# Kernel optimization log

Measured on AMD Instinct MI355X. Metric: run time of the kernel, lower is better.

The kernel has to match this reference:

```python
import jax, jax.numpy as jnp
import numpy as np

D_MODEL = 512
HEAD = 64

def setup_inputs() -> dict:
    key = jax.random.key(0)
    ks = jax.random.split(key, 7)
    s_in = 1.0 / np.sqrt(D_MODEL)
    x = jax.random.normal(ks[0], (4, 4096, D_MODEL), dtype=jnp.float32)
    Wk = jax.random.uniform(ks[1], (D_MODEL, HEAD), jnp.float32, -s_in, s_in)
    bk = jax.random.uniform(ks[2], (HEAD,), jnp.float32, -s_in, s_in)
    Wq = jax.random.uniform(ks[3], (D_MODEL, HEAD), jnp.float32, -s_in, s_in)
    bq = jax.random.uniform(ks[4], (HEAD,), jnp.float32, -s_in, s_in)
    Wv = jax.random.uniform(ks[5], (D_MODEL, HEAD), jnp.float32, -s_in, s_in)
    bv = jax.random.uniform(ks[6], (HEAD,), jnp.float32, -s_in, s_in)
    return {"x": x, "Wk": Wk, "bk": bk, "Wq": Wq, "bq": bq, "Wv": Wv, "bv": bv}

def reference(x, Wk, bk, Wq, bq, Wv, bv):
    B, T, C = x.shape
    k = x @ Wk + bk            # [B,T,H]
    q = x @ Wq + bq            # [B,T,H]
    v = x @ Wv + bv            # [B,T,H]
    scale = C ** (-0.5)
    # NOTE: original computes k @ q^T (keys index rows), softmax over query axis
    w = jnp.einsum('bkh,bqh->bkq', k, q) * scale  # [B,T,T]
    w = jax.nn.softmax(w, axis=-1)
    out = jnp.einsum('bkq,bqh->bkh', w, v)        # [B,T,H]
    return out
```

## Files before the change

### kernel.cpp

```cpp
#include <hip/hip_runtime.h>


#define DM 512
#define HD 64
#define TSEQ 4096
#define KSCALE (1.4426950408889634f * 0.04419417382415922f)

typedef __attribute__((ext_vector_type(8))) __bf16 bf16x8;
typedef __attribute__((ext_vector_type(4))) __bf16 bf16x4;
typedef __attribute__((ext_vector_type(2))) __bf16 bf16x2;
typedef __attribute__((ext_vector_type(4))) float f32x4;
typedef __attribute__((ext_vector_type(16))) float f32x16;
typedef __attribute__((ext_vector_type(4))) unsigned int uint4v;

__device__ __forceinline__ float fast_exp2(float x) {
#if __has_builtin(__builtin_amdgcn_exp2f)
    return __builtin_amdgcn_exp2f(x);
#else
    return exp2f(x);
#endif
}

__device__ __forceinline__ bf16x8 ld_bf16x8(const unsigned short* p) {
    return __builtin_bit_cast(bf16x8, *(const uint4v*)p);
}
__device__ __forceinline__ f32x4 mfma16(bf16x8 a, bf16x8 b, f32x4 c) {
    return __builtin_amdgcn_mfma_f32_16x16x32_bf16(a, b, c, 0, 0, 0);
}
__device__ __forceinline__ f32x16 mfma32(bf16x8 a, bf16x8 b, f32x16 c) {
    return __builtin_amdgcn_mfma_f32_32x32x16_bf16(a, b, c, 0, 0, 0);
}

typedef const __attribute__((address_space(1))) unsigned int* gas_t;
typedef __attribute__((address_space(3))) unsigned int* las_t;
__device__ __forceinline__ void async_cp16(const void* g, void* l) {
    __builtin_amdgcn_global_load_lds((gas_t)(unsigned long long)g,
                                     (las_t)(unsigned int)(unsigned long long)l,
                                     16, 0, 0);
}

__global__ __launch_bounds__(256) void prep_wt(const float* __restrict__ Wk,
                                               const float* __restrict__ Wq,
                                               const float* __restrict__ Wv,
                                               unsigned short* __restrict__ WT) {
    int e = blockIdx.x * 256 + threadIdx.x;
    int m = e >> 15;
    int idx = e & 32767;
    int h = idx >> 9;
    int cc = idx & 511;
    const float* W = (m == 0) ? Wk : ((m == 1) ? Wq : Wv);
    float v = W[cc * HD + h];
    if (m == 0) v *= KSCALE;
    ((__bf16*)WT)[m * 32768 + h * DM + cc] = (__bf16)v;
}

__global__ __launch_bounds__(512, 4) void proj(const float* __restrict__ x,
                                               const unsigned short* __restrict__ WT,
                                               const float* __restrict__ bk,
                                               const float* __restrict__ bq,
                                               const float* __restrict__ bv,
                                               unsigned short* __restrict__ Kw,
                                               unsigned short* __restrict__ Qw,
                                               unsigned short* __restrict__ VTw) {
    __shared__ alignas(16) float xs[16384];
    const int tid = threadIdx.x;
    const int wv = tid >> 6, lane = tid & 63;
    const int c = lane & 15, quad = lane >> 4;
    const int ng = wv & 3, rg = wv >> 2;
    const int bx = blockIdx.x;
    const int n0 = ng * 16;

#pragma unroll
    for (int r = 0; r < 8; ++r) {
        int cid = r * 512 + tid;
        int row = cid >> 7, pos = cid & 127;
        int g = (pos & ~7) | ((pos ^ row) & 7);
        async_cp16((const char*)x + (size_t)(bx * 32 + row) * 2048 + g * 16,
                   (char*)xs + r * 8192 + wv * 1024);
    }
    __builtin_amdgcn_s_waitcnt(0x0f70);
    __syncthreads();

    const int arow = rg * 16 + c;
    const unsigned short* wtb = WT + (n0 + c) * DM + quad * 8;
    f32x4 acc[3];
#pragma unroll
    for (int m = 0; m < 3; ++m) acc[m] = (f32x4){0.f, 0.f, 0.f, 0.f};

#pragma unroll
    for (int ks = 0; ks < 16; ++ks) {
        int p0 = ks * 8 + quad * 2;
        int sp0 = (p0 & ~7) | ((p0 ^ arow) & 7);
        int sp1 = ((p0 + 1) & ~7) | (((p0 + 1) ^ arow) & 7);
        f32x4 xa = *(const f32x4*)((const char*)xs + arow * 2048 + sp0 * 16);
        f32x4 xb = *(const f32x4*)((const char*)xs + arow * 2048 + sp1 * 16);
        bf16x8 af;
        af[0] = (__bf16)xa[0]; af[1] = (__bf16)xa[1]; af[2] = (__bf16)xa[2]; af[3] = (__bf16)xa[3];
        af[4] = (__bf16)xb[0]; af[5] = (__bf16)xb[1]; af[6] = (__bf16)xb[2]; af[7] = (__bf16)xb[3];
#pragma unroll
        for (int m = 0; m < 3; ++m) {
            bf16x8 bf = ld_bf16x8(wtb + m * 32768 + ks * 32);
            acc[m] = mfma16(af, bf, acc[m]);
        }
    }

    const int row0 = bx * 32 + rg * 16 + quad * 4;
#pragma unroll
    for (int m = 0; m < 3; ++m) {
        const float* bp = (m == 0) ? bk : ((m == 1) ? bq : bv);
        float bias = bp[n0 + c];
        if (m == 0) bias *= KSCALE;
        if (m < 2) {
            __bf16* dst = (__bf16*)((m == 0) ? Kw : Qw);
#pragma unroll
            for (int r = 0; r < 4; ++r)
                dst[(row0 + r) * HD + n0 + c] = (__bf16)(acc[m][r] + bias);
        } else {
            bf16x4 pk;
#pragma unroll
            for (int r = 0; r < 4; ++r) pk[r] = (__bf16)(acc[m][r] + bias);
            int b = bx >> 7;
            int rowb = (bx & 127) * 32 + rg * 16 + quad * 4;
            *(bf16x4*)(VTw + ((size_t)(b * 64 + n0 + c)) * TSEQ + rowb) = pk;
        }
    }
}

__global__ __launch_bounds__(512, 2) void attn(const unsigned short* __restrict__ Kw,
                                               const unsigned short* __restrict__ Qw,
                                               const unsigned short* __restrict__ VTw,
                                               float* __restrict__ Op,
                                               float* __restrict__ Lp) {
    __shared__ alignas(16) char smem[131072];

    const int tid = threadIdx.x;
    const int wv = tid >> 6, lane = tid & 63;
    const int l5 = lane >> 5, l31 = lane & 31;
    const int rg = wv >> 2, jc = wv & 3;
    const int bx = blockIdx.x;
    const int lb = (bx & 7) * 32 + (bx >> 3);
    const int batch = lb >> 6, js = (lb >> 5) & 1, tile = lb & 31;
    const int rowbase = batch * TSEQ + tile * 128;

    bf16x8 kf[2][4];
#pragma unroll
    for (int it = 0; it < 2; ++it) {
        const unsigned short* kp = Kw + (size_t)(rowbase + rg * 64 + it * 32 + l31) * HD;
#pragma unroll
        for (int ks = 0; ks < 4; ++ks) kf[it][ks] = ld_bf16x8(kp + ks * 16 + l5 * 8);
    }

    char* wbase = smem + wv * 16384;

    int qoff[4];
#pragma unroll
    for (int ks = 0; ks < 4; ++ks)
        qoff[ks] = l31 * 128 + (((ks * 2 + l5) ^ (l31 & 7)) * 16);
    int voff[2][2];
#pragma unroll
    for (int ht = 0; ht < 2; ++ht)
#pragma unroll
        for (int k2 = 0; k2 < 2; ++k2) {
            int h = ht * 32 + l31;
            int k = k2 * 2 + l5;
            voff[ht][k2] = h * 64 + (((k + h) & 3) * 16);
        }

    const char* qg = (const char*)(Qw + ((size_t)batch * TSEQ + js * 2048 + jc * 32) * HD);
    const char* vg = (const char*)(VTw + (size_t)batch * 64 * TSEQ) + js * 4096 + jc * 64;
    int qo[4], vo[4];
    {
        const int kk = ((lane & 3) + 4 - ((lane >> 2) & 3)) & 3;
#pragma unroll
        for (int op = 0; op < 4; ++op) {
            int r = (lane >> 3) + 8 * op;
            qo[op] = r * 128 + (((lane & 7) ^ (lane >> 3)) * 16);
            vo[op] = ((lane >> 2) + 16 * op) * 8192 + kk * 16;
        }
    }

    f32x16 o00, o01, o10, o11;
#pragma unroll
    for (int r = 0; r < 16; ++r) { o00[r] = 0.f; o01[r] = 0.f; o10[r] = 0.f; o11[r] = 0.f; }
    float lac0 = 0.f, lac1 = 0.f;

    auto STAGE = [&](int t) {
        char* nb = wbase + (t & 1) * 8192;
#pragma unroll
        for (int op = 0; op < 4; ++op)
            async_cp16(qg + t * 16384 + qo[op], nb + op * 1024);
#pragma unroll
        for (int op = 0; op < 4; ++op)
            async_cp16(vg + t * 256 + vo[op], nb + 4096 + op * 1024);
    };

    auto COMPUTE = [&](int jt) {
        const char* cb = wbase + (jt & 1) * 8192;
        const unsigned short* QL = (const unsigned short*)cb;
        const unsigned short* VL = (const unsigned short*)(cb + 4096);

        f32x16 s0, s1;
#pragma unroll
        for (int r = 0; r < 16; ++r) { s0[r] = 0.f; s1[r] = 0.f; }
#pragma unroll
        for (int ks = 0; ks < 4; ++ks) {
            bf16x8 qa = ld_bf16x8((const unsigned short*)((const char*)QL + qoff[ks]));
            s0 = mfma32(qa, kf[0][ks], s0);
            s1 = mfma32(qa, kf[1][ks], s1);
        }

        unsigned int pk0[8], pk1[8];
#pragma unroll
        for (int m = 0; m < 8; ++m) {
            float a0 = fast_exp2(s0[2 * m]), a1 = fast_exp2(s0[2 * m + 1]);
            float b0 = fast_exp2(s1[2 * m]), b1 = fast_exp2(s1[2 * m + 1]);
            lac0 += a0 + a1;
            lac1 += b0 + b1;
            bf16x2 ta; ta[0] = (__bf16)a0; ta[1] = (__bf16)a1;
            bf16x2 tb; tb[0] = (__bf16)b0; tb[1] = (__bf16)b1;
            pk0[m] = __builtin_bit_cast(unsigned int, ta);
            pk1[m] = __builtin_bit_cast(unsigned int, tb);
        }

#pragma unroll
        for (int k2 = 0; k2 < 2; ++k2) {
            bf16x8 pb0, pb1;
            {
                unsigned int A0 = pk0[k2 * 4 + 0], A1 = pk0[k2 * 4 + 1];
                unsigned int B0 = pk0[k2 * 4 + 2], B1 = pk0[k2 * 4 + 3];
                unsigned int t0 = l5 ? A0 : B0, t1 = l5 ? A1 : B1;
                unsigned int r0 = (unsigned int)__shfl_xor((int)t0, 32, 64);
                unsigned int r1 = (unsigned int)__shfl_xor((int)t1, 32, 64);
                uint4v u;
                u[0] = l5 ? r0 : A0; u[1] = l5 ? r1 : A1;
                u[2] = l5 ? B0 : r0; u[3] = l5 ? B1 : r1;
                pb0 = __builtin_bit_cast(bf16x8, u);
            }
            {
                unsigned int A0 = pk1[k2 * 4 + 0], A1 = pk1[k2 * 4 + 1];
                unsigned int B0 = pk1[k2 * 4 + 2], B1 = pk1[k2 * 4 + 3];
                unsigned int t0 = l5 ? A0 : B0, t1 = l5 ? A1 : B1;
                unsigned int r0 = (unsigned int)__shfl_xor((int)t0, 32, 64);
                unsigned int r1 = (unsigned int)__shfl_xor((int)t1, 32, 64);
                uint4v u;
                u[0] = l5 ? r0 : A0; u[1] = l5 ? r1 : A1;
                u[2] = l5 ? B0 : r0; u[3] = l5 ? B1 : r1;
                pb1 = __builtin_bit_cast(bf16x8, u);
            }
            bf16x8 vf0 = ld_bf16x8((const unsigned short*)((const char*)VL + voff[0][k2]));
            bf16x8 vf1 = ld_bf16x8((const unsigned short*)((const char*)VL + voff[1][k2]));
            o00 = mfma32(vf0, pb0, o00);
            o01 = mfma32(vf0, pb1, o01);
            o10 = mfma32(vf1, pb0, o10);
            o11 = mfma32(vf1, pb1, o11);
        }
    };

    __builtin_amdgcn_s_waitcnt(0x0f70);
    STAGE(0);
#pragma unroll 1
    for (int jt = 0; jt < 15; ++jt) {
        STAGE(jt + 1);
        __builtin_amdgcn_sched_barrier(0);
        __builtin_amdgcn_s_waitcnt(0x0f78);
        __builtin_amdgcn_sched_barrier(0);
        COMPUTE(jt);
    }
    __builtin_amdgcn_s_waitcnt(0x0f70);
    __builtin_amdgcn_sched_barrier(0);
    COMPUTE(15);

    lac0 += __shfl_xor(lac0, 32, 64);
    lac1 += __shfl_xor(lac1, 32, 64);
    __syncthreads();
    float* OCp = (float*)smem;
    float* ldsl = (float*)(smem + 34816);
    if (l5 == 0) {
        ldsl[jc * 128 + rg * 64 + l31] = lac0;
        ldsl[jc * 128 + rg * 64 + 32 + l31] = lac1;
    }

#pragma unroll
    for (int ph = 0; ph < 4; ++ph) {
        const int ht = ph >> 1, ih = ph & 1;
        __syncthreads();
        if (rg == ih) {
            const f32x16 oa = ht ? o10 : o00;
            const f32x16 ob = ht ? o11 : o01;
#pragma unroll
            for (int r = 0; r < 16; ++r) {
                int hr = (r & 3) + 8 * (r >> 2) + 4 * l5;
                OCp[(jc * 32 + hr) * 68 + l31] = oa[r];
                OCp[(jc * 32 + hr) * 68 + 32 + l31] = ob[r];
            }
        }
        __syncthreads();
#pragma unroll
        for (int rep = 0; rep < 4; ++rep) {
            int idx = rep * 512 + tid;
            int i = idx >> 5, hr = idx & 31;
            float v = OCp[(0 * 32 + hr) * 68 + i] + OCp[(1 * 32 + hr) * 68 + i]
                    + OCp[(2 * 32 + hr) * 68 + i] + OCp[(3 * 32 + hr) * 68 + i];
            Op[(size_t)js * 1048576 + (size_t)(rowbase + ih * 64 + i) * HD + ht * 32 + hr] = v;
        }
        if (ph == 0 && tid < 128) {
            float L = ldsl[tid] + ldsl[128 + tid] + ldsl[256 + tid] + ldsl[384 + tid];
            Lp[js * 16384 + rowbase + tid] = L;
        }
    }
}

__global__ __launch_bounds__(512) void fin(const float* __restrict__ Op,
                                           const float* __restrict__ Lp,
                                           float* __restrict__ out) {
    int idx = blockIdx.x * 512 + threadIdx.x;
    int e = idx * 4;
    int row = e >> 6;
    f32x4 a = *(const f32x4*)(Op + e);
    f32x4 b = *(const f32x4*)(Op + 1048576 + e);
    float L = Lp[row] + Lp[16384 + row];
    f32x4 r;
#pragma unroll
    for (int k = 0; k < 4; ++k) r[k] = (a[k] + b[k]) / L;
    *(f32x4*)(out + e) = r;
}

extern "C" void kernel_launch(void* const* d_in, const int* in_sizes, int n_in,
                              void* d_out, int out_size, void* d_ws, size_t ws_size,
                              hipStream_t stream) {
    (void)in_sizes; (void)n_in; (void)out_size; (void)ws_size;
    const float* x  = (const float*)d_in[0];
    const float* Wk = (const float*)d_in[1];
    const float* bk = (const float*)d_in[2];
    const float* Wq = (const float*)d_in[3];
    const float* bq = (const float*)d_in[4];
    const float* Wv = (const float*)d_in[5];
    const float* bv = (const float*)d_in[6];

    char* ws = (char*)d_ws;
    unsigned short* WT  = (unsigned short*)(ws);
    unsigned short* Kw  = (unsigned short*)(ws + 196608);
    unsigned short* Qw  = (unsigned short*)(ws + 2293760);
    unsigned short* VTw = (unsigned short*)(ws + 4390912);
    float* Opart        = (float*)(ws + 6488064);
    float* Lpart        = (float*)(ws + 14876672);
    float* outp = (float*)d_out;

    hipLaunchKernelGGL(prep_wt, dim3(384), dim3(256), 0, stream, Wk, Wq, Wv, WT);
    hipLaunchKernelGGL(proj, dim3(512), dim3(512), 0, stream,
                       x, WT, bk, bq, bv, Kw, Qw, VTw);
    hipLaunchKernelGGL(attn, dim3(256), dim3(512), 0, stream, Kw, Qw, VTw, Opart, Lpart);
    hipLaunchKernelGGL(fin, dim3(512), dim3(512), 0, stream, Opart, Lpart, outp);
}
```

Before: 137.1 us.

## Share block-wide double-buffered Q/V tiles across waves with syncthreads pipeline

Each wave used to stage its own private Q/V slice into its own LDS region and wait only on its own async copies. Now all waves stage a block-wide 256-column Q/V tile cooperatively into a shared double buffer, synchronize with __syncthreads, and each wave processes two 32-column sub-tiles per iteration over 8 iterations instead of 16. This halves loop trips and uses larger coalesced copies, at the cost of block-wide barriers and more LDS per buffer, which may lower occupancy.

```diff
diff --git a/kernel.cpp b/kernel.cpp
--- a/kernel.cpp
+++ b/kernel.cpp
@@ -150,33 +150,37 @@
         for (int ks = 0; ks < 4; ++ks) kf[it][ks] = ld_bf16x8(kp + ks * 16 + l5 * 8);
     }
 
-    char* wbase = smem + wv * 16384;
-
-    int qoff[4];
-#pragma unroll
-    for (int ks = 0; ks < 4; ++ks)
-        qoff[ks] = l31 * 128 + (((ks * 2 + l5) ^ (l31 & 7)) * 16);
-    int voff[2][2];
-#pragma unroll
-    for (int ht = 0; ht < 2; ++ht)
-#pragma unroll
-        for (int k2 = 0; k2 < 2; ++k2) {
-            int h = ht * 32 + l31;
-            int k = k2 * 2 + l5;
-            voff[ht][k2] = h * 64 + (((k + h) & 3) * 16);
-        }
-
-    const char* qg = (const char*)(Qw + ((size_t)batch * TSEQ + js * 2048 + jc * 32) * HD);
-    const char* vg = (const char*)(VTw + (size_t)batch * 64 * TSEQ) + js * 4096 + jc * 64;
-    int qo[4], vo[4];
-    {
-        const int kk = ((lane & 3) + 4 - ((lane >> 2) & 3)) & 3;
-#pragma unroll
-        for (int op = 0; op < 4; ++op) {
-            int r = (lane >> 3) + 8 * op;
-            qo[op] = r * 128 + (((lane & 7) ^ (lane >> 3)) * 16);
-            vo[op] = ((lane >> 2) + 16 * op) * 8192 + kk * 16;
-        }
+    int qoff[2][4];
+#pragma unroll
+    for (int jj = 0; jj < 2; ++jj) {
+        int jrow = jc * 64 + jj * 32 + l31;
+#pragma unroll
+        for (int ks = 0; ks < 4; ++ks)
+            qoff[jj][ks] = jrow * 128 + (((ks * 2 + l5) ^ (jrow & 7)) * 16);
+    }
+    int voff[2][2][2];
+#pragma unroll
+    for (int jj = 0; jj < 2; ++jj)
+#pragma unroll
+        for (int ht = 0; ht < 2; ++ht)
+#pragma unroll
+            for (int k2 = 0; k2 < 2; ++k2) {
+                int h = ht * 32 + l31;
+                int wc = (jc * 2 + jj) * 4 + k2 * 2 + l5;
+                int sc = (wc & 24) | ((wc ^ h) & 7);
+                voff[jj][ht][k2] = h * 512 + sc * 16;
+            }
+
+    const char* qg = (const char*)(Qw + (size_t)(batch * TSEQ + js * 2048) * HD);
+    const char* vg = (const char*)(VTw + (size_t)batch * 64 * TSEQ) + js * 4096;
+    int qgo[4], vgo[4];
+#pragma unroll
+    for (int op = 0; op < 4; ++op) {
+        int c = op * 512 + tid;
+        qgo[op] = ((c >> 3) * 128) + ((((c & 7) ^ (c >> 3)) & 7) * 16);
+        int vrow = c >> 5, sc = c & 31;
+        int wc = (sc & 24) | (((sc ^ vrow)) & 7);
+        vgo[op] = vrow * 8192 + wc * 16;
     }
 
     f32x16 o00, o01, o10, o11;
@@ -185,90 +189,88 @@
     float lac0 = 0.f, lac1 = 0.f;
 
     auto STAGE = [&](int t) {
-        char* nb = wbase + (t & 1) * 8192;
+        char* nb = smem + (t & 1) * 65536;
 #pragma unroll
         for (int op = 0; op < 4; ++op)
-            async_cp16(qg + t * 16384 + qo[op], nb + op * 1024);
+            async_cp16(qg + t * 32768 + qgo[op], nb + op * 8192 + wv * 1024);
 #pragma unroll
         for (int op = 0; op < 4; ++op)
-            async_cp16(vg + t * 256 + vo[op], nb + 4096 + op * 1024);
+            async_cp16(vg + t * 512 + vgo[op], nb + 32768 + op * 8192 + wv * 1024);
     };
 
-    auto COMPUTE = [&](int jt) {
-        const char* cb = wbase + (jt & 1) * 8192;
+    STAGE(0);
+
+#pragma unroll 1
+    for (int jt = 0; jt < 8; ++jt) {
+        __builtin_amdgcn_s_waitcnt(0x0f70);
+        __syncthreads();
+        const char* cb = smem + (jt & 1) * 65536;
+        if (jt < 7) {
+            STAGE(jt + 1);
+            __builtin_amdgcn_sched_barrier(0);
+        }
         const unsigned short* QL = (const unsigned short*)cb;
-        const unsigned short* VL = (const unsigned short*)(cb + 4096);
-
-        f32x16 s0, s1;
-#pragma unroll
-        for (int r = 0; r < 16; ++r) { s0[r] = 0.f; s1[r] = 0.f; }
-#pragma unroll
-        for (int ks = 0; ks < 4; ++ks) {
-            bf16x8 qa = ld_bf16x8((const unsigned short*)((const char*)QL + qoff[ks]));
-            s0 = mfma32(qa, kf[0][ks], s0);
-            s1 = mfma32(qa, kf[1][ks], s1);
-        }
-
-        unsigned int pk0[8], pk1[8];
-#pragma unroll
-        for (int m = 0; m < 8; ++m) {
-            float a0 = fast_exp2(s0[2 * m]), a1 = fast_exp2(s0[2 * m + 1]);
-            float b0 = fast_exp2(s1[2 * m]), b1 = fast_exp2(s1[2 * m + 1]);
-            lac0 += a0 + a1;
-            lac1 += b0 + b1;
-            bf16x2 ta; ta[0] = (__bf16)a0; ta[1] = (__bf16)a1;
-            bf16x2 tb; tb[0] = (__bf16)b0; tb[1] = (__bf16)b1;
-            pk0[m] = __builtin_bit_cast(unsigned int, ta);
-            pk1[m] = __builtin_bit_cast(unsigned int, tb);
-        }
-
-#pragma unroll
-        for (int k2 = 0; k2 < 2; ++k2) {
-            bf16x8 pb0, pb1;
-            {
-                unsigned int A0 = pk0[k2 * 4 + 0], A1 = pk0[k2 * 4 + 1];
-                unsigned int B0 = pk0[k2 * 4 + 2], B1 = pk0[k2 * 4 + 3];
-                unsigned int t0 = l5 ? A0 : B0, t1 = l5 ? A1 : B1;
-                unsigned int r0 = (unsigned int)__shfl_xor((int)t0, 32, 64);
-                unsigned int r1 = (unsigned int)__shfl_xor((int)t1, 32, 64);
-                uint4v u;
-                u[0] = l5 ? r0 : A0; u[1] = l5 ? r1 : A1;
-                u[2] = l5 ? B0 : r0; u[3] = l5 ? B1 : r1;
-                pb0 = __builtin_bit_cast(bf16x8, u);
-            }
-            {
-                unsigned int A0 = pk1[k2 * 4 + 0], A1 = pk1[k2 * 4 + 1];
-                unsigned int B0 = pk1[k2 * 4 + 2], B1 = pk1[k2 * 4 + 3];
-                unsigned int t0 = l5 ? A0 : B0, t1 = l5 ? A1 : B1;
-                unsigned int r0 = (unsigned int)__shfl_xor((int)t0, 32, 64);
-                unsigned int r1 = (unsigned int)__shfl_xor((int)t1, 32, 64);
-                uint4v u;
-                u[0] = l5 ? r0 : A0; u[1] = l5 ? r1 : A1;
-                u[2] = l5 ? B0 : r0; u[3] = l5 ? B1 : r1;
-                pb1 = __builtin_bit_cast(bf16x8, u);
-            }
-            bf16x8 vf0 = ld_bf16x8((const unsigned short*)((const char*)VL + voff[0][k2]));
-            bf16x8 vf1 = ld_bf16x8((const unsigned short*)((const char*)VL + voff[1][k2]));
-            o00 = mfma32(vf0, pb0, o00);
-            o01 = mfma32(vf0, pb1, o01);
-            o10 = mfma32(vf1, pb0, o10);
-            o11 = mfma32(vf1, pb1, o11);
-        }
-    };
-
-    __builtin_amdgcn_s_waitcnt(0x0f70);
-    STAGE(0);
-#pragma unroll 1
-    for (int jt = 0; jt < 15; ++jt) {
-        STAGE(jt + 1);
-        __builtin_amdgcn_sched_barrier(0);
-        __builtin_amdgcn_s_waitcnt(0x0f78);
-        __builtin_amdgcn_sched_barrier(0);
-        COMPUTE(jt);
-    }
-    __builtin_amdgcn_s_waitcnt(0x0f70);
-    __builtin_amdgcn_sched_barrier(0);
-    COMPUTE(15);
+        const unsigned short* VL = (const unsigned short*)(cb + 32768);
+
+#pragma unroll
+        for (int jj = 0; jj < 2; ++jj) {
+            f32x16 s0, s1;
+#pragma unroll
+            for (int r = 0; r < 16; ++r) { s0[r] = 0.f; s1[r] = 0.f; }
+#pragma unroll
+            for (int ks = 0; ks < 4; ++ks) {
+                bf16x8 qa = ld_bf16x8((const unsigned short*)((const char*)QL + qoff[jj][ks]));
+                s0 = mfma32(qa, kf[0][ks], s0);
+                s1 = mfma32(qa, kf[1][ks], s1);
+            }
+
+            unsigned int pk0[8], pk1[8];
+#pragma unroll
+            for (int m = 0; m < 8; ++m) {
+                float a0 = fast_exp2(s0[2 * m]), a1 = fast_exp2(s0[2 * m + 1]);
+                float b0 = fast_exp2(s1[2 * m]), b1 = fast_exp2(s1[2 * m + 1]);
+                lac0 += a0 + a1;
+                lac1 += b0 + b1;
+                bf16x2 ta; ta[0] = (__bf16)a0; ta[1] = (__bf16)a1;
+                bf16x2 tb; tb[0] = (__bf16)b0; tb[1] = (__bf16)b1;
+                pk0[m] = __builtin_bit_cast(unsigned int, ta);
+                pk1[m] = __builtin_bit_cast(unsigned int, tb);
+            }
+
+#pragma unroll
+            for (int k2 = 0; k2 < 2; ++k2) {
+                bf16x8 pb0, pb1;
+                {
+                    unsigned int A0 = pk0[k2 * 4 + 0], A1 = pk0[k2 * 4 + 1];
+                    unsigned int B0 = pk0[k2 * 4 + 2], B1 = pk0[k2 * 4 + 3];
+                    unsigned int t0 = l5 ? A0 : B0, t1 = l5 ? A1 : B1;
+                    unsigned int r0 = (unsigned int)__shfl_xor((int)t0, 32, 64);
+                    unsigned int r1 = (unsigned int)__shfl_xor((int)t1, 32, 64);
+                    uint4v u;
+                    u[0] = l5 ? r0 : A0; u[1] = l5 ? r1 : A1;
+                    u[2] = l5 ? B0 : r0; u[3] = l5 ? B1 : r1;
+                    pb0 = __builtin_bit_cast(bf16x8, u);
+                }
+                {
+                    unsigned int A0 = pk1[k2 * 4 + 0], A1 = pk1[k2 * 4 + 1];
+                    unsigned int B0 = pk1[k2 * 4 + 2], B1 = pk1[k2 * 4 + 3];
+                    unsigned int t0 = l5 ? A0 : B0, t1 = l5 ? A1 : B1;
+                    unsigned int r0 = (unsigned int)__shfl_xor((int)t0, 32, 64);
+                    unsigned int r1 = (unsigned int)__shfl_xor((int)t1, 32, 64);
+                    uint4v u;
+                    u[0] = l5 ? r0 : A0; u[1] = l5 ? r1 : A1;
+                    u[2] = l5 ? B0 : r0; u[3] = l5 ? B1 : r1;
+                    pb1 = __builtin_bit_cast(bf16x8, u);
+                }
+                bf16x8 vf0 = ld_bf16x8((const unsigned short*)((const char*)VL + voff[jj][0][k2]));
+                bf16x8 vf1 = ld_bf16x8((const unsigned short*)((const char*)VL + voff[jj][1][k2]));
+                o00 = mfma32(vf0, pb0, o00);
+                o01 = mfma32(vf0, pb1, o01);
+                o10 = mfma32(vf1, pb0, o10);
+                o11 = mfma32(vf1, pb1, o11);
+            }
+        }
+    }
 
     lac0 += __shfl_xor(lac0, 32, 64);
     lac1 += __shfl_xor(lac1, 32, 64);
```

After: 135.1 us. No clear change (-1.5%).
